# Performance work log

Hardware: AMD Instinct MI355X
Metric: run time of the kernel (lower is better)

Reference implementation:

```python
import jax, jax.numpy as jnp
import numpy as np

B, S, IN, OUT = 8, 4096, 1024, 1024


def setup_inputs() -> dict:
    key = jax.random.key(0)
    k1, k2, k3, k4, k5 = jax.random.split(key, 5)
    x = jax.random.normal(k1, (B, S, IN), dtype=jnp.float32)
    # pre-quantized int8 weight buffer [out, in]
    weight = jax.random.randint(k2, (OUT, IN), -127, 128, dtype=jnp.int32).astype(jnp.int8)
    bias = jax.random.normal(k3, (OUT,), dtype=jnp.float32) * 0.1
    # per-channel weight clip values (>0)
    w_clip_val = jax.random.uniform(k4, (OUT,), minval=0.5, maxval=2.0, dtype=jnp.float32)
    # smoothquant per-input-channel activation scaling factors (>0)
    smoothquant_scale = jax.random.uniform(k5, (IN,), minval=0.5, maxval=2.0, dtype=jnp.float32)
    return {"x": x, "weight": weight, "bias": bias,
            "w_clip_val": w_clip_val, "smoothquant_scale": smoothquant_scale}


def reference(x, weight, bias, w_clip_val, smoothquant_scale):
    # i8i8_aiu semantics for weight_quant_type='per_channel',
    # activ_quant_type='per_token' (symmetric -> zero_shift == 0), smoothquant=True.
    # 1) smoothquant: scale activations prior to quantization
    xs = x / smoothquant_scale                                   # [B,S,IN]
    # 2) per-token symmetric int8 quantization of activations
    a_scale = jnp.max(jnp.abs(xs), axis=-1, keepdims=True) / 127.0  # [B,S,1]
    a_scale = jnp.maximum(a_scale, 1e-8)
    x_int = jnp.round(jnp.clip(xs / a_scale, -127.0, 127.0)).astype(jnp.int8)
    acc = jax.lax.dot_general(x_int, weight,
                              dimension_numbers=(((2,), (1,)), ((), ())),
                              preferred_element_type=jnp.int32)
    # 4) fused dequant (per-token act scale * per-channel weight scale) + bias
    w_scale = w_clip_val / 127.0                                 # [OUT]
    return acc.astype(jnp.float32) * a_scale * w_scale + bias
```

## Files before the change

kernel.cpp:

```cpp
#include <hip/hip_runtime.h>
#include <stdint.h>

#define T_TOK 32768
#define NIN   1024
#define NOUT  1024
#define BM    32
#define NTHR  512

typedef int v4i  __attribute__((ext_vector_type(4)));
typedef int v16i __attribute__((ext_vector_type(16)));

__global__ __launch_bounds__(256) void repack_w_frag(const int* __restrict__ w,
                                                     uint32_t* __restrict__ wf) {
  const int gid  = blockIdx.x * 256 + threadIdx.x;
  const int lane = gid & 63;
  const int ks   = (gid >> 6) & 31;
  const int nt   = gid >> 11;
  const int n    = nt * 32 + (lane & 31);
  const int kb   = ks * 32 + (lane >> 5) * 16;
  const int* src = w + (size_t)n * NIN + kb;
  uint32_t d[4];
#pragma unroll
  for (int q = 0; q < 4; ++q) {
    const int4 v = ((const int4*)src)[q];
    d[q] = (uint32_t)(v.x & 0xff) | ((uint32_t)(v.y & 0xff) << 8) |
           ((uint32_t)(v.z & 0xff) << 16) | ((uint32_t)(v.w & 0xff) << 24);
  }
  ((uint4*)wf)[gid] = make_uint4(d[0], d[1], d[2], d[3]);
}

__global__ __launch_bounds__(NTHR) void fused_w8a8(
    const float* __restrict__ x,
    const uint8_t* __restrict__ wf,
    const float* __restrict__ sq,
    const float* __restrict__ wclip,
    const float* __restrict__ bias,
    float* __restrict__ out)
{
  __shared__ __align__(16) uint8_t A8[BM * NIN];
  __shared__ float ascale_s[BM];

  const int tid  = threadIdx.x;
  const int lane = tid & 63;
  const int w    = tid >> 6;
  const int t0   = blockIdx.x * BM;

  const float4* sq4 = (const float4*)sq;
  float4 rs[4];
#pragma unroll
  for (int j = 0; j < 4; ++j) {
    const float4 s = sq4[j * 64 + lane];
    rs[j].x = __builtin_amdgcn_rcpf(s.x);
    rs[j].y = __builtin_amdgcn_rcpf(s.y);
    rs[j].z = __builtin_amdgcn_rcpf(s.z);
    rs[j].w = __builtin_amdgcn_rcpf(s.w);
  }
#pragma unroll
  for (int i = 0; i < 4; ++i) {
    const int tl = w * 4 + i;
    const float4* xr = (const float4*)(x + (size_t)(t0 + tl) * NIN);
    float4 v[4];
    float m = 0.f;
#pragma unroll
    for (int j = 0; j < 4; ++j) {
      float4 a = xr[j * 64 + lane];
      a.x *= rs[j].x; a.y *= rs[j].y; a.z *= rs[j].z; a.w *= rs[j].w;
      v[j] = a;
      m = fmaxf(m, fmaxf(fmaxf(fabsf(a.x), fabsf(a.y)),
                         fmaxf(fabsf(a.z), fabsf(a.w))));
    }
#pragma unroll
    for (int off = 1; off < 64; off <<= 1) m = fmaxf(m, __shfl_xor(m, off));
    const float as = fmaxf(m * (1.f / 127.f), 1e-8f);
    if (lane == 0) ascale_s[tl] = as;
    const float ia = __builtin_amdgcn_rcpf(as);
#pragma unroll
    for (int j = 0; j < 4; ++j) {
      const int q0 = (int)rintf(fminf(fmaxf(v[j].x * ia, -127.f), 127.f));
      const int q1 = (int)rintf(fminf(fmaxf(v[j].y * ia, -127.f), 127.f));
      const int q2 = (int)rintf(fminf(fmaxf(v[j].z * ia, -127.f), 127.f));
      const int q3 = (int)rintf(fminf(fmaxf(v[j].w * ia, -127.f), 127.f));
      const uint32_t d = (uint32_t)(q0 & 0xff) | ((uint32_t)(q1 & 0xff) << 8) |
                         ((uint32_t)(q2 & 0xff) << 16) | ((uint32_t)(q3 & 0xff) << 24);
      const int di = j * 64 + lane;
      const int ch = (di >> 2) ^ (tl & 7);
      *(uint32_t*)(A8 + tl * NIN + ch * 16 + (di & 3) * 4) = d;
    }
  }
  __syncthreads();

  v16i acc[4] = {};

  auto ldB = [&](int ks, int nt) -> v4i {
    return *(const v4i*)(wf +
        ((((size_t)(w * 4 + nt) * 32 + ks) * 64 + lane) << 4));
  };
  auto ldA = [&](int ks) -> v4i {
    const int row = lane & 31;
    const int ch  = (ks * 2 + (lane >> 5)) ^ (row & 7);
    return *(const v4i*)(A8 + row * NIN + ch * 16);
  };

  v4i B[4][4];
#pragma unroll
  for (int p = 0; p < 4; ++p)
#pragma unroll
    for (int nt = 0; nt < 4; ++nt) B[p][nt] = ldB(p, nt);

  for (int ks = 0; ks < 32; ks += 4) {
#pragma unroll
    for (int p = 0; p < 4; ++p) {
      const v4i af = ldA(ks + p);
#pragma unroll
      for (int nt = 0; nt < 4; ++nt)
        acc[nt] = __builtin_amdgcn_mfma_i32_32x32x32_i8(af, B[p][nt], acc[nt], 0, 0, 0);
      if (ks + 4 + p < 32) {
#pragma unroll
        for (int nt = 0; nt < 4; ++nt) B[p][nt] = ldB(ks + 4 + p, nt);
      }
    }
  }

#pragma unroll
  for (int nt = 0; nt < 4; ++nt) {
    const int n = (w * 4 + nt) * 32 + (lane & 31);
    const float wsc = wclip[n] * (1.f / 127.f);
    const float bs  = bias[n];
#pragma unroll
    for (int reg = 0; reg < 16; ++reg) {
      const int r = (reg & 3) + 8 * (reg >> 2) + 4 * (lane >> 5);
      out[(size_t)(t0 + r) * NOUT + n] =
          (float)acc[nt][reg] * ascale_s[r] * wsc + bs;
    }
  }
}

extern "C" void kernel_launch(void* const* d_in, const int* in_sizes, int n_in,
                              void* d_out, int out_size, void* d_ws, size_t ws_size,
                              hipStream_t stream) {
  const float* x      = (const float*)d_in[0];
  const int*   weight = (const int*)d_in[1];
  const float* bias   = (const float*)d_in[2];
  const float* wclip  = (const float*)d_in[3];
  const float* sq     = (const float*)d_in[4];
  float* out = (float*)d_out;

  uint32_t* wfrag = (uint32_t*)d_ws;

  repack_w_frag<<<(NOUT * NIN / 16) / 256, 256, 0, stream>>>(weight, wfrag);
  fused_w8a8<<<T_TOK / BM, NTHR, 0, stream>>>(x, (const uint8_t*)wfrag,
                                              sq, wclip, bias, out);
}
```

Before: 92.10 us.

## Double token tile to 64 rows with 2x2 MFMA warp tiles

Result: faster. 80.05 us (-13.1%).

```diff
diff --git a/kernel.cpp b/kernel.cpp
--- a/kernel.cpp
+++ b/kernel.cpp
@@ -4,8 +4,8 @@
 #define T_TOK 32768
 #define NIN   1024
 #define NOUT  1024
-#define BM    32
-#define NTHR  512
+#define BM    64
+#define NTHR  1024
 
 typedef int v4i  __attribute__((ext_vector_type(4)));
 typedef int v16i __attribute__((ext_vector_type(16)));
@@ -29,110 +29,129 @@
   ((uint4*)wf)[gid] = make_uint4(d[0], d[1], d[2], d[3]);
 }
 
-__global__ __launch_bounds__(NTHR) void fused_w8a8(
+__global__ __launch_bounds__(NTHR, 1) void fused_w8a8(
     const float* __restrict__ x,
     const uint8_t* __restrict__ wf,
     const float* __restrict__ sq,
     const float* __restrict__ wclip,
     const float* __restrict__ bias,
+    float* __restrict__ asc_g,
     float* __restrict__ out)
 {
-  __shared__ __align__(16) uint8_t A8[BM * NIN];
-  __shared__ float ascale_s[BM];
+  __shared__ __align__(16) uint8_t Af[BM * NIN];
 
   const int tid  = threadIdx.x;
   const int lane = tid & 63;
   const int w    = tid >> 6;
   const int t0   = blockIdx.x * BM;
 
-  const float4* sq4 = (const float4*)sq;
-  float4 rs[4];
-#pragma unroll
-  for (int j = 0; j < 4; ++j) {
-    const float4 s = sq4[j * 64 + lane];
-    rs[j].x = __builtin_amdgcn_rcpf(s.x);
-    rs[j].y = __builtin_amdgcn_rcpf(s.y);
-    rs[j].z = __builtin_amdgcn_rcpf(s.z);
-    rs[j].w = __builtin_amdgcn_rcpf(s.w);
-  }
-#pragma unroll
-  for (int i = 0; i < 4; ++i) {
-    const int tl = w * 4 + i;
-    const float4* xr = (const float4*)(x + (size_t)(t0 + tl) * NIN);
-    float4 v[4];
-    float m = 0.f;
+  const uint8_t* wfw = wf + (((size_t)w * 2) * 32 * 64) * 16;
+  auto ldB = [&](int ks, int j) -> v4i {
+    return *(const v4i*)(wfw + ((((j * 32 + ks) * 64) + lane) << 4));
+  };
+  v4i Ba0 = ldB(0, 0), Ba1 = ldB(0, 1);
+  v4i Bb0 = ldB(1, 0), Bb1 = ldB(1, 1);
+
+  {
+    const float4* sq4 = (const float4*)sq;
+    float4 rs[4];
 #pragma unroll
     for (int j = 0; j < 4; ++j) {
-      float4 a = xr[j * 64 + lane];
-      a.x *= rs[j].x; a.y *= rs[j].y; a.z *= rs[j].z; a.w *= rs[j].w;
-      v[j] = a;
-      m = fmaxf(m, fmaxf(fmaxf(fabsf(a.x), fabsf(a.y)),
-                         fmaxf(fabsf(a.z), fabsf(a.w))));
+      const float4 s = sq4[j * 64 + lane];
+      rs[j].x = __builtin_amdgcn_rcpf(s.x);
+      rs[j].y = __builtin_amdgcn_rcpf(s.y);
+      rs[j].z = __builtin_amdgcn_rcpf(s.z);
+      rs[j].w = __builtin_amdgcn_rcpf(s.w);
     }
 #pragma unroll
-    for (int off = 1; off < 64; off <<= 1) m = fmaxf(m, __shfl_xor(m, off));
-    const float as = fmaxf(m * (1.f / 127.f), 1e-8f);
-    if (lane == 0) ascale_s[tl] = as;
-    const float ia = __builtin_amdgcn_rcpf(as);
+    for (int i = 0; i < 4; ++i) {
+      const int tl = w * 4 + i;
+      const float4* xr = (const float4*)(x + (size_t)(t0 + tl) * NIN);
+      float4 v[4];
+      float m = 0.f;
 #pragma unroll
-    for (int j = 0; j < 4; ++j) {
-      const int q0 = (int)rintf(fminf(fmaxf(v[j].x * ia, -127.f), 127.f));
-      const int q1 = (int)rintf(fminf(fmaxf(v[j].y * ia, -127.f), 127.f));
-      const int q2 = (int)rintf(fminf(fmaxf(v[j].z * ia, -127.f), 127.f));
-      const int q3 = (int)rintf(fminf(fmaxf(v[j].w * ia, -127.f), 127.f));
-      const uint32_t d = (uint32_t)(q0 & 0xff) | ((uint32_t)(q1 & 0xff) << 8) |
-                         ((uint32_t)(q2 & 0xff) << 16) | ((uint32_t)(q3 & 0xff) << 24);
-      const int di = j * 64 + lane;
-      const int ch = (di >> 2) ^ (tl & 7);
-      *(uint32_t*)(A8 + tl * NIN + ch * 16 + (di & 3) * 4) = d;
+      for (int j = 0; j < 4; ++j) {
+        float4 a = xr[j * 64 + lane];
+        a.x *= rs[j].x; a.y *= rs[j].y; a.z *= rs[j].z; a.w *= rs[j].w;
+        v[j] = a;
+        m = fmaxf(m, fmaxf(fmaxf(fabsf(a.x), fabsf(a.y)),
+                           fmaxf(fabsf(a.z), fabsf(a.w))));
+      }
+#pragma unroll
+      for (int off = 1; off < 64; off <<= 1) m = fmaxf(m, __shfl_xor(m, off));
+      const float as = fmaxf(m * (1.f / 127.f), 1e-8f);
+      if (lane == 0) asc_g[t0 + tl] = as;
+      const float ia = __builtin_amdgcn_rcpf(as);
+      const int mt = tl >> 5;
+#pragma unroll
+      for (int j = 0; j < 4; ++j) {
+        const int q0 = (int)rintf(fminf(fmaxf(v[j].x * ia, -127.f), 127.f));
+        const int q1 = (int)rintf(fminf(fmaxf(v[j].y * ia, -127.f), 127.f));
+        const int q2 = (int)rintf(fminf(fmaxf(v[j].z * ia, -127.f), 127.f));
+        const int q3 = (int)rintf(fminf(fmaxf(v[j].w * ia, -127.f), 127.f));
+        const uint32_t d = (uint32_t)(q0 & 0xff) | ((uint32_t)(q1 & 0xff) << 8) |
+                           ((uint32_t)(q2 & 0xff) << 16) | ((uint32_t)(q3 & 0xff) << 24);
+        const int di  = j * 64 + lane;
+        const int ksw = di >> 3;
+        const int h   = (di >> 2) & 1;
+        const int slot = (tl & 31) + 32 * h;
+        const int chunk = (mt * 32 + ksw) * 64 + (slot ^ (ksw & 7));
+        *(uint32_t*)(Af + chunk * 16 + (di & 3) * 4) = d;
+      }
     }
   }
   __syncthreads();
 
-  v16i acc[4] = {};
-
-  auto ldB = [&](int ks, int nt) -> v4i {
-    return *(const v4i*)(wf +
-        ((((size_t)(w * 4 + nt) * 32 + ks) * 64 + lane) << 4));
-  };
-  auto ldA = [&](int ks) -> v4i {
-    const int row = lane & 31;
-    const int ch  = (ks * 2 + (lane >> 5)) ^ (row & 7);
-    return *(const v4i*)(A8 + row * NIN + ch * 16);
+  auto ldA = [&](int mt, int ks) -> v4i {
+    return *(const v4i*)(Af + ((((mt * 32 + ks) * 64) + (lane ^ (ks & 7))) << 4));
   };
 
-  v4i B[4][4];
-#pragma unroll
-  for (int p = 0; p < 4; ++p)
-#pragma unroll
-    for (int nt = 0; nt < 4; ++nt) B[p][nt] = ldB(p, nt);
+  v16i acc00 = {}, acc01 = {}, acc10 = {}, acc11 = {};
 
-  for (int ks = 0; ks < 32; ks += 4) {
-#pragma unroll
-    for (int p = 0; p < 4; ++p) {
-      const v4i af = ldA(ks + p);
-#pragma unroll
-      for (int nt = 0; nt < 4; ++nt)
-        acc[nt] = __builtin_amdgcn_mfma_i32_32x32x32_i8(af, B[p][nt], acc[nt], 0, 0, 0);
-      if (ks + 4 + p < 32) {
-#pragma unroll
-        for (int nt = 0; nt < 4; ++nt) B[p][nt] = ldB(ks + 4 + p, nt);
-      }
+  for (int ks = 0; ks < 32; ks += 2) {
+    {
+      const v4i a0 = ldA(0, ks), a1 = ldA(1, ks);
+      __builtin_amdgcn_s_setprio(1);
+      acc00 = __builtin_amdgcn_mfma_i32_32x32x32_i8(a0, Ba0, acc00, 0, 0, 0);
+      acc01 = __builtin_amdgcn_mfma_i32_32x32x32_i8(a0, Ba1, acc01, 0, 0, 0);
+      acc10 = __builtin_amdgcn_mfma_i32_32x32x32_i8(a1, Ba0, acc10, 0, 0, 0);
+      acc11 = __builtin_amdgcn_mfma_i32_32x32x32_i8(a1, Ba1, acc11, 0, 0, 0);
+      __builtin_amdgcn_s_setprio(0);
+      if (ks + 2 < 32) { Ba0 = ldB(ks + 2, 0); Ba1 = ldB(ks + 2, 1); }
+    }
+    {
+      const v4i a0 = ldA(0, ks + 1), a1 = ldA(1, ks + 1);
+      __builtin_amdgcn_s_setprio(1);
+      acc00 = __builtin_amdgcn_mfma_i32_32x32x32_i8(a0, Bb0, acc00, 0, 0, 0);
+      acc01 = __builtin_amdgcn_mfma_i32_32x32x32_i8(a0, Bb1, acc01, 0, 0, 0);
+      acc10 = __builtin_amdgcn_mfma_i32_32x32x32_i8(a1, Bb0, acc10, 0, 0, 0);
+      acc11 = __builtin_amdgcn_mfma_i32_32x32x32_i8(a1, Bb1, acc11, 0, 0, 0);
+      __builtin_amdgcn_s_setprio(0);
+      if (ks + 3 < 32) { Bb0 = ldB(ks + 3, 0); Bb1 = ldB(ks + 3, 1); }
     }
   }
 
-#pragma unroll
-  for (int nt = 0; nt < 4; ++nt) {
-    const int n = (w * 4 + nt) * 32 + (lane & 31);
-    const float wsc = wclip[n] * (1.f / 127.f);
-    const float bs  = bias[n];
-#pragma unroll
-    for (int reg = 0; reg < 16; ++reg) {
-      const int r = (reg & 3) + 8 * (reg >> 2) + 4 * (lane >> 5);
-      out[(size_t)(t0 + r) * NOUT + n] =
-          (float)acc[nt][reg] * ascale_s[r] * wsc + bs;
-    }
-  }
+  const int hr = 4 * (lane >> 5);
+  const float* ascw = asc_g + t0;
+
+#define EPI(ACC, MT, NTL)                                                    \
+  do {                                                                       \
+    const int n = w * 64 + (NTL) * 32 + (lane & 31);                         \
+    const float wsc = wclip[n] * (1.f / 127.f);                              \
+    const float bs  = bias[n];                                               \
+    _Pragma("unroll")                                                        \
+    for (int reg = 0; reg < 16; ++reg) {                                     \
+      const int r = (MT) * 32 + (reg & 3) + 8 * (reg >> 2) + hr;             \
+      out[(size_t)(t0 + r) * NOUT + n] =                                     \
+          (float)ACC[reg] * ascw[r] * wsc + bs;                              \
+    }                                                                        \
+  } while (0)
+
+  EPI(acc00, 0, 0);
+  EPI(acc01, 0, 1);
+  EPI(acc10, 1, 0);
+  EPI(acc11, 1, 1);
+#undef EPI
 }
 
 extern "C" void kernel_launch(void* const* d_in, const int* in_sizes, int n_in,
@@ -146,8 +165,9 @@
   float* out = (float*)d_out;
 
   uint32_t* wfrag = (uint32_t*)d_ws;
+  float*    asc_g = (float*)((uint8_t*)d_ws + (size_t)(NOUT / 32) * 32 * 64 * 16);
 
   repack_w_frag<<<(NOUT * NIN / 16) / 256, 256, 0, stream>>>(weight, wfrag);
   fused_w8a8<<<T_TOK / BM, NTHR, 0, stream>>>(x, (const uint8_t*)wfrag,
-                                              sq, wclip, bias, out);
+                                              sq, wclip, bias, asc_g, out);
 }
```

## Double-buffer quantized activation tiles and overlap next-tile quantization with MFMA GEMM

Applied to the files above, without the earlier changes.

Result: slower. 136.4 us (+48.1%).

```diff
diff --git a/kernel.cpp b/kernel.cpp
--- a/kernel.cpp
+++ b/kernel.cpp
@@ -1,14 +1,17 @@
 #include <hip/hip_runtime.h>
 #include <stdint.h>
 
-#define T_TOK 32768
-#define NIN   1024
-#define NOUT  1024
-#define BM    32
-#define NTHR  512
+#define T_TOK  32768
+#define NIN    1024
+#define NOUT   1024
+#define BM     64
+#define NTILES 2
+#define NTHR   512
 
 typedef int v4i  __attribute__((ext_vector_type(4)));
 typedef int v16i __attribute__((ext_vector_type(16)));
+
+#define MFMA_I8(a, b, c) __builtin_amdgcn_mfma_i32_32x32x32_i8(a, b, c, 0, 0, 0)
 
 __global__ __launch_bounds__(256) void repack_w_frag(const int* __restrict__ w,
                                                      uint32_t* __restrict__ wf) {
@@ -29,7 +32,7 @@
   ((uint4*)wf)[gid] = make_uint4(d[0], d[1], d[2], d[3]);
 }
 
-__global__ __launch_bounds__(NTHR) void fused_w8a8(
+__global__ __launch_bounds__(NTHR, 2) void fused_w8a8(
     const float* __restrict__ x,
     const uint8_t* __restrict__ wf,
     const float* __restrict__ sq,
@@ -37,102 +40,178 @@
     const float* __restrict__ bias,
     float* __restrict__ out)
 {
-  __shared__ __align__(16) uint8_t A8[BM * NIN];
-  __shared__ float ascale_s[BM];
-
-  const int tid  = threadIdx.x;
-  const int lane = tid & 63;
-  const int w    = tid >> 6;
-  const int t0   = blockIdx.x * BM;
-
-  const float4* sq4 = (const float4*)sq;
-  float4 rs[4];
-#pragma unroll
-  for (int j = 0; j < 4; ++j) {
-    const float4 s = sq4[j * 64 + lane];
-    rs[j].x = __builtin_amdgcn_rcpf(s.x);
-    rs[j].y = __builtin_amdgcn_rcpf(s.y);
-    rs[j].z = __builtin_amdgcn_rcpf(s.z);
-    rs[j].w = __builtin_amdgcn_rcpf(s.w);
-  }
-#pragma unroll
-  for (int i = 0; i < 4; ++i) {
-    const int tl = w * 4 + i;
-    const float4* xr = (const float4*)(x + (size_t)(t0 + tl) * NIN);
-    float4 v[4];
+  __shared__ __align__(16) uint8_t Af[2][BM * NIN];
+  __shared__ float ascale_s[2][BM];
+
+  const int tid    = threadIdx.x;
+  const int lane   = tid & 63;
+  const int w      = tid >> 6;
+  const int base_t = blockIdx.x * (BM * NTILES);
+
+  const uint8_t* wfw = wf + ((size_t)(w * 4) * 32 * 64) * 16;
+
+  v16i acc[2][4] = {};
+  v4i  Ba[4], Bb[4];
+  float4 xq0[4], xq1[4];
+  int qt0 = 0, qt1 = 0;
+
+  auto ldB = [&](int ks, int nt) -> v4i {
+    return *(const v4i*)(wfw + ((((nt * 32 + ks) * 64) + lane) << 4));
+  };
+  auto ldA = [&](int bufi, int mt, int ks, int ksl) -> v4i {
+    return *(const v4i*)(&Af[bufi][(((mt * 32 + ks) * 64) + (lane ^ ksl)) << 4]);
+  };
+
+  auto issue_group = [&](int tile_t0, int g) {
+    qt0 = w * 8 + g * 2;
+    qt1 = qt0 + 1;
+    const float4* xr0 = (const float4*)(x + (size_t)(tile_t0 + qt0) * NIN);
+    const float4* xr1 = (const float4*)(x + (size_t)(tile_t0 + qt1) * NIN);
+#pragma unroll
+    for (int j = 0; j < 4; ++j) {
+      xq0[j] = xr0[j * 64 + lane];
+      xq1[j] = xr1[j * 64 + lane];
+    }
+  };
+
+  auto quant_one = [&](int nbuf, int tl, const float4* vraw, const float4* rs) {
+    float4 sv[4];
     float m = 0.f;
 #pragma unroll
     for (int j = 0; j < 4; ++j) {
-      float4 a = xr[j * 64 + lane];
+      float4 a = vraw[j];
       a.x *= rs[j].x; a.y *= rs[j].y; a.z *= rs[j].z; a.w *= rs[j].w;
-      v[j] = a;
+      sv[j] = a;
       m = fmaxf(m, fmaxf(fmaxf(fabsf(a.x), fabsf(a.y)),
                          fmaxf(fabsf(a.z), fabsf(a.w))));
     }
 #pragma unroll
     for (int off = 1; off < 64; off <<= 1) m = fmaxf(m, __shfl_xor(m, off));
     const float as = fmaxf(m * (1.f / 127.f), 1e-8f);
-    if (lane == 0) ascale_s[tl] = as;
+    if (lane == 0) ascale_s[nbuf][tl] = as;
     const float ia = __builtin_amdgcn_rcpf(as);
-#pragma unroll
-    for (int j = 0; j < 4; ++j) {
-      const int q0 = (int)rintf(fminf(fmaxf(v[j].x * ia, -127.f), 127.f));
-      const int q1 = (int)rintf(fminf(fmaxf(v[j].y * ia, -127.f), 127.f));
-      const int q2 = (int)rintf(fminf(fmaxf(v[j].z * ia, -127.f), 127.f));
-      const int q3 = (int)rintf(fminf(fmaxf(v[j].w * ia, -127.f), 127.f));
+    const int mt = tl >> 5;
+#pragma unroll
+    for (int j = 0; j < 4; ++j) {
+      const int q0 = (int)rintf(fminf(fmaxf(sv[j].x * ia, -127.f), 127.f));
+      const int q1 = (int)rintf(fminf(fmaxf(sv[j].y * ia, -127.f), 127.f));
+      const int q2 = (int)rintf(fminf(fmaxf(sv[j].z * ia, -127.f), 127.f));
+      const int q3 = (int)rintf(fminf(fmaxf(sv[j].w * ia, -127.f), 127.f));
       const uint32_t d = (uint32_t)(q0 & 0xff) | ((uint32_t)(q1 & 0xff) << 8) |
                          ((uint32_t)(q2 & 0xff) << 16) | ((uint32_t)(q3 & 0xff) << 24);
-      const int di = j * 64 + lane;
-      const int ch = (di >> 2) ^ (tl & 7);
-      *(uint32_t*)(A8 + tl * NIN + ch * 16 + (di & 3) * 4) = d;
-    }
+      const int di   = j * 64 + lane;
+      const int ksw  = di >> 3;
+      const int h    = (di >> 2) & 1;
+      const int slot = (tl & 31) + 32 * h;
+      const int chunk = (mt * 32 + ksw) * 64 + (slot ^ (ksw & 7));
+      *(uint32_t*)(&Af[nbuf][chunk * 16 + (di & 3) * 4]) = d;
+    }
+  };
+
+  auto finish_group = [&](int nbuf) {
+    const float4* sq4 = (const float4*)sq;
+    float4 rs[4];
+#pragma unroll
+    for (int j = 0; j < 4; ++j) {
+      const float4 s = sq4[j * 64 + lane];
+      rs[j].x = __builtin_amdgcn_rcpf(s.x);
+      rs[j].y = __builtin_amdgcn_rcpf(s.y);
+      rs[j].z = __builtin_amdgcn_rcpf(s.z);
+      rs[j].w = __builtin_amdgcn_rcpf(s.w);
+    }
+    quant_one(nbuf, qt0, xq0, rs);
+    quant_one(nbuf, qt1, xq1, rs);
+  };
+
+#define GEMM8(BUF, KS0)                                                      \
+  do {                                                                       \
+    _Pragma("unroll")                                                        \
+    for (int c = 0; c < 8; c += 2) {                                         \
+      {                                                                      \
+        const v4i a0 = ldA(BUF, 0, (KS0) + c, c);                            \
+        const v4i a1 = ldA(BUF, 1, (KS0) + c, c);                            \
+        __builtin_amdgcn_s_setprio(1);                                       \
+        _Pragma("unroll")                                                    \
+        for (int nt = 0; nt < 4; ++nt) {                                     \
+          acc[0][nt] = MFMA_I8(a0, Ba[nt], acc[0][nt]);                      \
+          acc[1][nt] = MFMA_I8(a1, Ba[nt], acc[1][nt]);                      \
+        }                                                                    \
+        __builtin_amdgcn_s_setprio(0);                                       \
+        if ((KS0) + c + 2 < 32) {                                            \
+          _Pragma("unroll")                                                  \
+          for (int nt = 0; nt < 4; ++nt) Ba[nt] = ldB((KS0) + c + 2, nt);    \
+        }                                                                    \
+      }                                                                      \
+      {                                                                      \
+        const v4i a0 = ldA(BUF, 0, (KS0) + c + 1, c + 1);                    \
+        const v4i a1 = ldA(BUF, 1, (KS0) + c + 1, c + 1);                    \
+        __builtin_amdgcn_s_setprio(1);                                       \
+        _Pragma("unroll")                                                    \
+        for (int nt = 0; nt < 4; ++nt) {                                     \
+          acc[0][nt] = MFMA_I8(a0, Bb[nt], acc[0][nt]);                      \
+          acc[1][nt] = MFMA_I8(a1, Bb[nt], acc[1][nt]);                      \
+        }                                                                    \
+        __builtin_amdgcn_s_setprio(0);                                       \
+        if ((KS0) + c + 3 < 32) {                                            \
+          _Pragma("unroll")                                                  \
+          for (int nt = 0; nt < 4; ++nt) Bb[nt] = ldB((KS0) + c + 3, nt);    \
+        }                                                                    \
+      }                                                                      \
+    }                                                                        \
+  } while (0)
+
+  for (int g = 0; g < 4; ++g) {
+    issue_group(base_t, g);
+    finish_group(0);
   }
   __syncthreads();
 
-  v16i acc[4] = {};
-
-  auto ldB = [&](int ks, int nt) -> v4i {
-    return *(const v4i*)(wf +
-        ((((size_t)(w * 4 + nt) * 32 + ks) * 64 + lane) << 4));
-  };
-  auto ldA = [&](int ks) -> v4i {
-    const int row = lane & 31;
-    const int ch  = (ks * 2 + (lane >> 5)) ^ (row & 7);
-    return *(const v4i*)(A8 + row * NIN + ch * 16);
-  };
-
-  v4i B[4][4];
-#pragma unroll
-  for (int p = 0; p < 4; ++p)
-#pragma unroll
-    for (int nt = 0; nt < 4; ++nt) B[p][nt] = ldB(p, nt);
-
-  for (int ks = 0; ks < 32; ks += 4) {
-#pragma unroll
-    for (int p = 0; p < 4; ++p) {
-      const v4i af = ldA(ks + p);
-#pragma unroll
-      for (int nt = 0; nt < 4; ++nt)
-        acc[nt] = __builtin_amdgcn_mfma_i32_32x32x32_i8(af, B[p][nt], acc[nt], 0, 0, 0);
-      if (ks + 4 + p < 32) {
-#pragma unroll
-        for (int nt = 0; nt < 4; ++nt) B[p][nt] = ldB(ks + 4 + p, nt);
+#pragma unroll
+  for (int it = 0; it < NTILES; ++it) {
+    const int buf  = it & 1;
+    const int nbuf = buf ^ 1;
+    const int t0   = base_t + it * BM;
+    const bool has_next = (it + 1 < NTILES);
+    const int next_t0 = t0 + BM;
+
+#pragma unroll
+    for (int nt = 0; nt < 4; ++nt) { Ba[nt] = ldB(0, nt); Bb[nt] = ldB(1, nt); }
+
+    if (has_next) issue_group(next_t0, 0);
+    GEMM8(buf, 0);
+    if (has_next) { finish_group(nbuf); issue_group(next_t0, 1); }
+    GEMM8(buf, 8);
+    if (has_next) { finish_group(nbuf); issue_group(next_t0, 2); }
+    GEMM8(buf, 16);
+    if (has_next) { finish_group(nbuf); issue_group(next_t0, 3); }
+    GEMM8(buf, 24);
+    if (has_next) finish_group(nbuf);
+
+#pragma unroll
+    for (int mt = 0; mt < 2; ++mt) {
+      float ascv[16];
+#pragma unroll
+      for (int reg = 0; reg < 16; ++reg)
+        ascv[reg] =
+            ascale_s[buf][mt * 32 + (reg & 3) + 8 * (reg >> 2) + 4 * (lane >> 5)];
+#pragma unroll
+      for (int nt = 0; nt < 4; ++nt) {
+        const int n = w * 128 + nt * 32 + (lane & 31);
+        const float wsc = wclip[n] * (1.f / 127.f);
+        const float bs  = bias[n];
+#pragma unroll
+        for (int reg = 0; reg < 16; ++reg) {
+          const int r = mt * 32 + (reg & 3) + 8 * (reg >> 2) + 4 * (lane >> 5);
+          out[(size_t)(t0 + r) * NOUT + n] =
+              (float)acc[mt][nt][reg] * ascv[reg] * wsc + bs;
+        }
+#pragma unroll
+        for (int reg = 0; reg < 16; ++reg) acc[mt][nt][reg] = 0;
       }
     }
+    __syncthreads();
   }
-
-#pragma unroll
-  for (int nt = 0; nt < 4; ++nt) {
-    const int n = (w * 4 + nt) * 32 + (lane & 31);
-    const float wsc = wclip[n] * (1.f / 127.f);
-    const float bs  = bias[n];
-#pragma unroll
-    for (int reg = 0; reg < 16; ++reg) {
-      const int r = (reg & 3) + 8 * (reg >> 2) + 4 * (lane >> 5);
-      out[(size_t)(t0 + r) * NOUT + n] =
-          (float)acc[nt][reg] * ascale_s[r] * wsc + bs;
-    }
-  }
+#undef GEMM8
 }
 
 extern "C" void kernel_launch(void* const* d_in, const int* in_sizes, int n_in,
@@ -148,6 +227,6 @@
   uint32_t* wfrag = (uint32_t*)d_ws;
 
   repack_w_frag<<<(NOUT * NIN / 16) / 256, 256, 0, stream>>>(weight, wfrag);
-  fused_w8a8<<<T_TOK / BM, NTHR, 0, stream>>>(x, (const uint8_t*)wfrag,
-                                              sq, wclip, bias, out);
+  fused_w8a8<<<T_TOK / (BM * NTILES), NTHR, 0, stream>>>(
+      x, (const uint8_t*)wfrag, sq, wclip, bias, out);
 }
```

## Split quantization into separate fragment-layout kernel and tile GEMM over 128x128 blocks

Applied to the files above, without the earlier changes.

Measured after the change: 100.6 us. 1.09x slower.

```diff
diff --git a/kernel.cpp b/kernel.cpp
--- a/kernel.cpp
+++ b/kernel.cpp
@@ -4,11 +4,13 @@
 #define T_TOK 32768
 #define NIN   1024
 #define NOUT  1024
-#define BM    32
-#define NTHR  512
 
-typedef int v4i  __attribute__((ext_vector_type(4)));
-typedef int v16i __attribute__((ext_vector_type(16)));
+typedef int   v4i  __attribute__((ext_vector_type(4)));
+typedef int   v16i __attribute__((ext_vector_type(16)));
+typedef float v4f  __attribute__((ext_vector_type(4)));
+
+#define MFMA_I8(a, b, c) __builtin_amdgcn_mfma_i32_32x32x32_i8(a, b, c, 0, 0, 0)
+
 
 __global__ __launch_bounds__(256) void repack_w_frag(const int* __restrict__ w,
                                                      uint32_t* __restrict__ wf) {
@@ -29,108 +31,132 @@
   ((uint4*)wf)[gid] = make_uint4(d[0], d[1], d[2], d[3]);
 }
 
-__global__ __launch_bounds__(NTHR) void fused_w8a8(
-    const float* __restrict__ x,
+__global__ __launch_bounds__(256) void quant_frag(const float* __restrict__ x,
+                                                  const float* __restrict__ sq,
+                                                  uint32_t* __restrict__ afw,
+                                                  float* __restrict__ asc) {
+  const int lane = threadIdx.x & 63;
+  const int wid  = threadIdx.x >> 6;
+  const int tok  = blockIdx.x * 4 + wid;
+  const v4f* xr = (const v4f*)(x + (size_t)tok * NIN);
+  const v4f* sr = (const v4f*)sq;
+
+  v4f xs[4];
+  float m = 0.f;
+#pragma unroll
+  for (int j = 0; j < 4; ++j) {
+    const int idx = j * 64 + lane;
+    v4f xv = __builtin_nontemporal_load(&xr[idx]);
+    const v4f sv = sr[idx];
+    xv.x *= __builtin_amdgcn_rcpf(sv.x);
+    xv.y *= __builtin_amdgcn_rcpf(sv.y);
+    xv.z *= __builtin_amdgcn_rcpf(sv.z);
+    xv.w *= __builtin_amdgcn_rcpf(sv.w);
+    xs[j] = xv;
+    m = fmaxf(m, fmaxf(fmaxf(fabsf(xv.x), fabsf(xv.y)),
+                       fmaxf(fabsf(xv.z), fabsf(xv.w))));
+  }
+#pragma unroll
+  for (int off = 1; off < 64; off <<= 1) m = fmaxf(m, __shfl_xor(m, off));
+
+  const float a_scale = fmaxf(m * (1.f / 127.f), 1e-8f);
+  if (lane == 0) asc[tok] = a_scale;
+  const float inv_a = __builtin_amdgcn_rcpf(a_scale);
+
+  const int M = tok >> 5;
+  const int r = tok & 31;
+#pragma unroll
+  for (int j = 0; j < 4; ++j) {
+    const v4f v = xs[j];
+    const int q0 = (int)rintf(fminf(fmaxf(v.x * inv_a, -127.f), 127.f));
+    const int q1 = (int)rintf(fminf(fmaxf(v.y * inv_a, -127.f), 127.f));
+    const int q2 = (int)rintf(fminf(fmaxf(v.z * inv_a, -127.f), 127.f));
+    const int q3 = (int)rintf(fminf(fmaxf(v.w * inv_a, -127.f), 127.f));
+    const uint32_t d = (uint32_t)(q0 & 0xff) | ((uint32_t)(q1 & 0xff) << 8) |
+                       ((uint32_t)(q2 & 0xff) << 16) | ((uint32_t)(q3 & 0xff) << 24);
+    const int di = j * 64 + lane;
+    const int ks = di >> 3;
+    const int h  = (di >> 2) & 1;
+    const int chunk = (M * 32 + ks) * 64 + r + 32 * h;
+    afw[chunk * 4 + (di & 3)] = d;
+  }
+}
+
+__global__ __launch_bounds__(256, 3) void gemm_frag(
+    const uint8_t* __restrict__ af,
     const uint8_t* __restrict__ wf,
-    const float* __restrict__ sq,
+    const float* __restrict__ asc,
     const float* __restrict__ wclip,
     const float* __restrict__ bias,
     float* __restrict__ out)
 {
-  __shared__ __align__(16) uint8_t A8[BM * NIN];
-  __shared__ float ascale_s[BM];
+  const int g   = blockIdx.x;
+  const int xcd = g & 7;
+  const int j   = g >> 3;
+  const int T   = xcd * 32 + (j >> 3);
+  const int nb  = j & 7;
 
   const int tid  = threadIdx.x;
   const int lane = tid & 63;
   const int w    = tid >> 6;
-  const int t0   = blockIdx.x * BM;
+  const int wr   = w >> 1, wc = w & 1;
 
-  const float4* sq4 = (const float4*)sq;
-  float4 rs[4];
-#pragma unroll
-  for (int j = 0; j < 4; ++j) {
-    const float4 s = sq4[j * 64 + lane];
-    rs[j].x = __builtin_amdgcn_rcpf(s.x);
-    rs[j].y = __builtin_amdgcn_rcpf(s.y);
-    rs[j].z = __builtin_amdgcn_rcpf(s.z);
-    rs[j].w = __builtin_amdgcn_rcpf(s.w);
-  }
-#pragma unroll
-  for (int i = 0; i < 4; ++i) {
-    const int tl = w * 4 + i;
-    const float4* xr = (const float4*)(x + (size_t)(t0 + tl) * NIN);
-    float4 v[4];
-    float m = 0.f;
-#pragma unroll
-    for (int j = 0; j < 4; ++j) {
-      float4 a = xr[j * 64 + lane];
-      a.x *= rs[j].x; a.y *= rs[j].y; a.z *= rs[j].z; a.w *= rs[j].w;
-      v[j] = a;
-      m = fmaxf(m, fmaxf(fmaxf(fabsf(a.x), fabsf(a.y)),
-                         fmaxf(fabsf(a.z), fabsf(a.w))));
-    }
-#pragma unroll
-    for (int off = 1; off < 64; off <<= 1) m = fmaxf(m, __shfl_xor(m, off));
-    const float as = fmaxf(m * (1.f / 127.f), 1e-8f);
-    if (lane == 0) ascale_s[tl] = as;
-    const float ia = __builtin_amdgcn_rcpf(as);
-#pragma unroll
-    for (int j = 0; j < 4; ++j) {
-      const int q0 = (int)rintf(fminf(fmaxf(v[j].x * ia, -127.f), 127.f));
-      const int q1 = (int)rintf(fminf(fmaxf(v[j].y * ia, -127.f), 127.f));
-      const int q2 = (int)rintf(fminf(fmaxf(v[j].z * ia, -127.f), 127.f));
-      const int q3 = (int)rintf(fminf(fmaxf(v[j].w * ia, -127.f), 127.f));
-      const uint32_t d = (uint32_t)(q0 & 0xff) | ((uint32_t)(q1 & 0xff) << 8) |
-                         ((uint32_t)(q2 & 0xff) << 16) | ((uint32_t)(q3 & 0xff) << 24);
-      const int di = j * 64 + lane;
-      const int ch = (di >> 2) ^ (tl & 7);
-      *(uint32_t*)(A8 + tl * NIN + ch * 16 + (di & 3) * 4) = d;
-    }
-  }
-  __syncthreads();
+  const uint8_t* Ab = af + ((size_t)(T * 4 + wr * 2) << 15) + lane * 16;
+  const uint8_t* Bb = wf + ((size_t)(nb * 4 + wc * 2) << 15) + lane * 16;
 
-  v16i acc[4] = {};
-
-  auto ldB = [&](int ks, int nt) -> v4i {
-    return *(const v4i*)(wf +
-        ((((size_t)(w * 4 + nt) * 32 + ks) * 64 + lane) << 4));
+  auto ldA = [&](int mti, int ks) -> v4i {
+    return *(const v4i*)(Ab + mti * 32768 + ks * 1024);
   };
-  auto ldA = [&](int ks) -> v4i {
-    const int row = lane & 31;
-    const int ch  = (ks * 2 + (lane >> 5)) ^ (row & 7);
-    return *(const v4i*)(A8 + row * NIN + ch * 16);
+  auto ldB = [&](int nti, int ks) -> v4i {
+    return *(const v4i*)(Bb + nti * 32768 + ks * 1024);
   };
 
-  v4i B[4][4];
+  v16i acc[2][2] = {};
+  v4i Ar[4][2], Br[4][2];
 #pragma unroll
-  for (int p = 0; p < 4; ++p)
+  for (int p = 0; p < 4; ++p) {
+    Ar[p][0] = ldA(0, p); Ar[p][1] = ldA(1, p);
+    Br[p][0] = ldB(0, p); Br[p][1] = ldB(1, p);
+  }
+
 #pragma unroll
-    for (int nt = 0; nt < 4; ++nt) B[p][nt] = ldB(p, nt);
-
-  for (int ks = 0; ks < 32; ks += 4) {
-#pragma unroll
-    for (int p = 0; p < 4; ++p) {
-      const v4i af = ldA(ks + p);
-#pragma unroll
-      for (int nt = 0; nt < 4; ++nt)
-        acc[nt] = __builtin_amdgcn_mfma_i32_32x32x32_i8(af, B[p][nt], acc[nt], 0, 0, 0);
-      if (ks + 4 + p < 32) {
-#pragma unroll
-        for (int nt = 0; nt < 4; ++nt) B[p][nt] = ldB(ks + 4 + p, nt);
-      }
+  for (int ks = 0; ks < 32; ++ks) {
+    const int p = ks & 3;
+    const v4i a0 = Ar[p][0], a1 = Ar[p][1];
+    const v4i b0 = Br[p][0], b1 = Br[p][1];
+    __builtin_amdgcn_s_setprio(1);
+    acc[0][0] = MFMA_I8(a0, b0, acc[0][0]);
+    acc[0][1] = MFMA_I8(a0, b1, acc[0][1]);
+    acc[1][0] = MFMA_I8(a1, b0, acc[1][0]);
+    acc[1][1] = MFMA_I8(a1, b1, acc[1][1]);
+    __builtin_amdgcn_s_setprio(0);
+    if (ks < 28) {
+      Ar[p][0] = ldA(0, ks + 4); Ar[p][1] = ldA(1, ks + 4);
+      Br[p][0] = ldB(0, ks + 4); Br[p][1] = ldB(1, ks + 4);
     }
   }
 
+  const int t0 = T * 128 + wr * 64;
+  const int nbase = nb * 128 + wc * 64;
+  const int hr = 4 * (lane >> 5);
 #pragma unroll
-  for (int nt = 0; nt < 4; ++nt) {
-    const int n = (w * 4 + nt) * 32 + (lane & 31);
-    const float wsc = wclip[n] * (1.f / 127.f);
-    const float bs  = bias[n];
+  for (int mt = 0; mt < 2; ++mt) {
+    float ascv[16];
 #pragma unroll
-    for (int reg = 0; reg < 16; ++reg) {
-      const int r = (reg & 3) + 8 * (reg >> 2) + 4 * (lane >> 5);
-      out[(size_t)(t0 + r) * NOUT + n] =
-          (float)acc[nt][reg] * ascale_s[r] * wsc + bs;
+    for (int reg = 0; reg < 16; ++reg)
+      ascv[reg] = asc[t0 + mt * 32 + (reg & 3) + 8 * (reg >> 2) + hr];
+#pragma unroll
+    for (int nt = 0; nt < 2; ++nt) {
+      const int n = nbase + nt * 32 + (lane & 31);
+      const float wsc = wclip[n] * (1.f / 127.f);
+      const float bs  = bias[n];
+#pragma unroll
+      for (int reg = 0; reg < 16; ++reg) {
+        const int rrow = t0 + mt * 32 + (reg & 3) + 8 * (reg >> 2) + hr;
+        __builtin_nontemporal_store(
+            (float)acc[mt][nt][reg] * ascv[reg] * wsc + bs,
+            &out[(size_t)rrow * NOUT + n]);
+      }
     }
   }
 }
@@ -145,9 +171,14 @@
   const float* sq     = (const float*)d_in[4];
   float* out = (float*)d_out;
 
-  uint32_t* wfrag = (uint32_t*)d_ws;
+  uint8_t* ws = (uint8_t*)d_ws;
+  uint32_t* wfrag = (uint32_t*)ws;
+  uint32_t* afrag = (uint32_t*)(ws + (1u << 20));
+  float*    asc   = (float*)(ws + (1u << 20) + ((size_t)T_TOK * NIN));
 
   repack_w_frag<<<(NOUT * NIN / 16) / 256, 256, 0, stream>>>(weight, wfrag);
-  fused_w8a8<<<T_TOK / BM, NTHR, 0, stream>>>(x, (const uint8_t*)wfrag,
-                                              sq, wclip, bias, out);
+  quant_frag<<<T_TOK / 4, 256, 0, stream>>>(x, sq, afrag, asc);
+  gemm_frag<<<2048, 256, 0, stream>>>((const uint8_t*)afrag,
+                                      (const uint8_t*)wfrag,
+                                      asc, wclip, bias, out);
 }
```
